# Kernel optimization log

Measured on AMD Instinct MI355X. Metric: run time of the kernel, lower is better.

The kernel has to match this reference:

```python
import jax, jax.numpy as jnp
import numpy as np

NUM_SUPERPIXELS = 256


def setup_inputs() -> dict:
    key = jax.random.key(0)
    k1, k2 = jax.random.split(key)
    B, H, W, C = 8, 512, 512, 64
    feature_map = jax.random.normal(k1, (B, H, W, C), dtype=jnp.float32)
    superpixel_map = jax.random.randint(k2, (B, H, W), 0, NUM_SUPERPIXELS, dtype=jnp.int32)
    return {"feature_map": feature_map, "superpixel_map": superpixel_map}


def reference(feature_map, superpixel_map):
    # feature_map: [B,H,W,C] float; superpixel_map: [B,H,W] int labels in [0, S)
    B, H, W, C = feature_map.shape
    S = NUM_SUPERPIXELS
    num_segments = B * S
    feat = feature_map.reshape(-1, C)                       # [B*H*W, C]
    batch_ids = jnp.arange(B, dtype=jnp.int32)[:, None, None]
    seg = (batch_ids * S + superpixel_map).reshape(-1)      # global segment id [B*H*W]
    sums = jax.ops.segment_sum(feat, seg, num_segments=num_segments)          # [B*S, C]
    counts = jax.ops.segment_sum(jnp.ones((seg.shape[0],), feat.dtype), seg,
                                 num_segments=num_segments)                    # [B*S]
    means = sums / jnp.maximum(counts, 1.0)[:, None]        # empty segments -> 0
    return means.reshape(B, S, C)
```

## Files before the change

kernel.cpp:

```cpp
#include <hip/hip_runtime.h>


#define NBATCH 8
#define NSEG 256
#define NCH 64
#define PPB (512 * 512)
#define BLOCKS_PER_BATCH 64
#define PIX_PER_BLOCK 4096
#define NWAVE 8
#define NCHUNK 16
#define CHUNK_PIX 256
#define QMAX 256
#define NROWS (NSEG + NWAVE)

__global__ __launch_bounds__(512, 4) void pool_kernel(const float* __restrict__ feat,
                                                      const int* __restrict__ sp,
                                                      float* __restrict__ outsum,
                                                      unsigned* __restrict__ cnts) {
    __shared__ float hist[NROWS * NCH];
    __shared__ unsigned cnt[NROWS];
    __shared__ int qd[NWAVE][QMAX];

    const int b = blockIdx.x >> 6;
    const int slab = blockIdx.x & 63;
    const int tid = threadIdx.x;
    const int lane = tid & 63;
    const int wave = tid >> 6;

    for (int i = tid; i < NROWS * NCH; i += 512) hist[i] = 0.0f;
    if (tid < NROWS) cnt[tid] = 0u;
    __syncthreads();

    const int pixbase = slab * PIX_PER_BLOCK;
    const int4* lp4 = (const int4*)(sp + (size_t)b * PPB + pixbase);
    const float* fb = feat + ((size_t)b * PPB + pixbase) * NCH + lane;

    const int dummy_e = (NSEG + wave) << 12;
    int* q = qd[wave];

    int4 lab = lp4[lane];
    for (int c = 0; c < NCHUNK; ++c) {
        const int cn = (c + 1 < NCHUNK) ? (c + 1) : c;
        int4 nlab = lp4[cn * 64 + lane];
        int qn = 0;
        const int pbase = c * CHUNK_PIX + 4 * lane;

#define PUSH(SV, CC)                                                          \
        {                                                                     \
            const int s_ = (SV);                                              \
            const bool own_ = ((s_ >> 5) == wave);                            \
            const unsigned long long m_ = __ballot(own_);                     \
            if (own_) {                                                       \
                const int r_ = __builtin_amdgcn_mbcnt_hi(                     \
                    (unsigned)(m_ >> 32),                                     \
                    __builtin_amdgcn_mbcnt_lo((unsigned)m_, 0));              \
                q[qn + r_] = (s_ << 12) | (pbase + (CC));                     \
            }                                                                 \
            qn += __builtin_popcountll(m_);                                   \
        }
        PUSH(lab.x, 0) PUSH(lab.y, 1) PUSH(lab.z, 2) PUSH(lab.w, 3)
#undef PUSH

        const int npad = (4 - (qn & 3)) & 3;
        if (lane < npad) q[qn + lane] = dummy_e;
        qn += npad;

        const int ng = qn >> 2;
        if (ng) {
            int4 eA = *(const int4*)&q[0];
            float fA0 = fb[(size_t)(eA.x & 4095) * NCH];
            float fA1 = fb[(size_t)(eA.y & 4095) * NCH];
            float fA2 = fb[(size_t)(eA.z & 4095) * NCH];
            float fA3 = fb[(size_t)(eA.w & 4095) * NCH];
            for (int g = 1; g < ng; ++g) {
                int4 eB = *(const int4*)&q[g * 4];
                float fB0 = fb[(size_t)(eB.x & 4095) * NCH];
                float fB1 = fb[(size_t)(eB.y & 4095) * NCH];
                float fB2 = fb[(size_t)(eB.z & 4095) * NCH];
                float fB3 = fb[(size_t)(eB.w & 4095) * NCH];

                hist[(eA.x >> 12) * NCH + lane] += fA0;
                if (lane == 0) cnt[eA.x >> 12]++;
                hist[(eA.y >> 12) * NCH + lane] += fA1;
                if (lane == 0) cnt[eA.y >> 12]++;
                hist[(eA.z >> 12) * NCH + lane] += fA2;
                if (lane == 0) cnt[eA.z >> 12]++;
                hist[(eA.w >> 12) * NCH + lane] += fA3;
                if (lane == 0) cnt[eA.w >> 12]++;

                eA = eB; fA0 = fB0; fA1 = fB1; fA2 = fB2; fA3 = fB3;
            }
            hist[(eA.x >> 12) * NCH + lane] += fA0;
            if (lane == 0) cnt[eA.x >> 12]++;
            hist[(eA.y >> 12) * NCH + lane] += fA1;
            if (lane == 0) cnt[eA.y >> 12]++;
            hist[(eA.z >> 12) * NCH + lane] += fA2;
            if (lane == 0) cnt[eA.z >> 12]++;
            hist[(eA.w >> 12) * NCH + lane] += fA3;
            if (lane == 0) cnt[eA.w >> 12]++;
        }
        lab = nlab;
    }
    __syncthreads();

    const size_t obase = (size_t)b * NSEG * NCH;
    for (int i = tid; i < NSEG * NCH; i += 512)
        unsafeAtomicAdd(&outsum[obase + i], hist[i]);
    if (tid < NSEG) atomicAdd(&cnts[(size_t)b * NSEG + tid], cnt[tid]);
}

__global__ void init_kernel(float* __restrict__ outsum, unsigned* __restrict__ cnts) {
    const int i = blockIdx.x * 256 + threadIdx.x;
    ((float4*)outsum)[i] = make_float4(0.f, 0.f, 0.f, 0.f);
    if (i < (NBATCH * NSEG) / 4) ((uint4*)cnts)[i] = make_uint4(0u, 0u, 0u, 0u);
}

__global__ void finalize_kernel(float* __restrict__ outsum,
                                const unsigned* __restrict__ cnts) {
    const int idx4 = blockIdx.x * blockDim.x + threadIdx.x;
    const unsigned c = cnts[idx4 >> 4];
    const float inv = 1.0f / (float)(c > 0u ? c : 1u);
    float4 v = ((float4*)outsum)[idx4];
    v.x *= inv; v.y *= inv; v.z *= inv; v.w *= inv;
    ((float4*)outsum)[idx4] = v;
}

extern "C" void kernel_launch(void* const* d_in, const int* in_sizes, int n_in,
                              void* d_out, int out_size, void* d_ws, size_t ws_size,
                              hipStream_t stream) {
    const float* feat = (const float*)d_in[0];
    const int* sp = (const int*)d_in[1];
    float* out = (float*)d_out;
    unsigned* cnts = (unsigned*)d_ws;
    (void)in_sizes; (void)n_in; (void)out_size; (void)ws_size;

    init_kernel<<<512, 256, 0, stream>>>(out, cnts);
    pool_kernel<<<NBATCH * BLOCKS_PER_BATCH, 512, 0, stream>>>(feat, sp, out, cnts);
    finalize_kernel<<<(NBATCH * NSEG * NCH / 4) / 256, 256, 0, stream>>>(out, cnts);
}
```

Baseline: 706.2 us.

## Replace global atomics with per-block partials and a separate reduce kernel

Each block now writes its shared-memory histogram and counts to its own workspace slot instead of atomically adding into the output. A new reduce kernel sums the 64 partials per batch and segment and divides by the count, which removes the init and finalize kernels. Counts are now taken with shared atomics at push time instead of per gathered element, and the gather loop is unrolled to 8 loads in flight. Launch bounds drop to 2 blocks per CU. The change trades global atomic contention for about 32 MB of extra workspace traffic plus a second pass, and relies on the workspace being large enough.

```diff
diff --git a/kernel.cpp b/kernel.cpp
--- a/kernel.cpp
+++ b/kernel.cpp
@@ -5,18 +5,18 @@
 #define NSEG 256
 #define NCH 64
 #define PPB (512 * 512)
-#define BLOCKS_PER_BATCH 64
+#define BPB 64
 #define PIX_PER_BLOCK 4096
 #define NWAVE 8
 #define NCHUNK 16
 #define CHUNK_PIX 256
-#define QMAX 256
+#define QMAX 264
 #define NROWS (NSEG + NWAVE)
 
-__global__ __launch_bounds__(512, 4) void pool_kernel(const float* __restrict__ feat,
+__global__ __launch_bounds__(512, 2) void pool_kernel(const float* __restrict__ feat,
                                                       const int* __restrict__ sp,
-                                                      float* __restrict__ outsum,
-                                                      unsigned* __restrict__ cnts) {
+                                                      float* __restrict__ pspart,
+                                                      unsigned* __restrict__ pscnt) {
     __shared__ float hist[NROWS * NCH];
     __shared__ unsigned cnt[NROWS];
     __shared__ int qd[NWAVE][QMAX];
@@ -27,7 +27,8 @@
     const int lane = tid & 63;
     const int wave = tid >> 6;
 
-    for (int i = tid; i < NROWS * NCH; i += 512) hist[i] = 0.0f;
+    for (int i = tid; i < (NROWS * NCH) / 4; i += 512)
+        ((float4*)hist)[i] = make_float4(0.f, 0.f, 0.f, 0.f);
     if (tid < NROWS) cnt[tid] = 0u;
     __syncthreads();
 
@@ -55,74 +56,91 @@
                     (unsigned)(m_ >> 32),                                     \
                     __builtin_amdgcn_mbcnt_lo((unsigned)m_, 0));              \
                 q[qn + r_] = (s_ << 12) | (pbase + (CC));                     \
+                atomicAdd(&cnt[s_], 1u);                                      \
             }                                                                 \
             qn += __builtin_popcountll(m_);                                   \
         }
         PUSH(lab.x, 0) PUSH(lab.y, 1) PUSH(lab.z, 2) PUSH(lab.w, 3)
 #undef PUSH
 
-        const int npad = (4 - (qn & 3)) & 3;
+        const int npad = (8 - (qn & 7)) & 7;
         if (lane < npad) q[qn + lane] = dummy_e;
         qn += npad;
 
-        const int ng = qn >> 2;
+        const int ng = qn >> 3;
         if (ng) {
-            int4 eA = *(const int4*)&q[0];
-            float fA0 = fb[(size_t)(eA.x & 4095) * NCH];
-            float fA1 = fb[(size_t)(eA.y & 4095) * NCH];
-            float fA2 = fb[(size_t)(eA.z & 4095) * NCH];
-            float fA3 = fb[(size_t)(eA.w & 4095) * NCH];
+            int4 a0 = *(const int4*)&q[0];
+            int4 a1 = *(const int4*)&q[4];
+            float f0 = fb[(size_t)(a0.x & 4095) * NCH];
+            float f1 = fb[(size_t)(a0.y & 4095) * NCH];
+            float f2 = fb[(size_t)(a0.z & 4095) * NCH];
+            float f3 = fb[(size_t)(a0.w & 4095) * NCH];
+            float f4 = fb[(size_t)(a1.x & 4095) * NCH];
+            float f5 = fb[(size_t)(a1.y & 4095) * NCH];
+            float f6 = fb[(size_t)(a1.z & 4095) * NCH];
+            float f7 = fb[(size_t)(a1.w & 4095) * NCH];
             for (int g = 1; g < ng; ++g) {
-                int4 eB = *(const int4*)&q[g * 4];
-                float fB0 = fb[(size_t)(eB.x & 4095) * NCH];
-                float fB1 = fb[(size_t)(eB.y & 4095) * NCH];
-                float fB2 = fb[(size_t)(eB.z & 4095) * NCH];
-                float fB3 = fb[(size_t)(eB.w & 4095) * NCH];
+                int4 b0 = *(const int4*)&q[g * 8];
+                int4 b1 = *(const int4*)&q[g * 8 + 4];
+                float h0 = fb[(size_t)(b0.x & 4095) * NCH];
+                float h1 = fb[(size_t)(b0.y & 4095) * NCH];
+                float h2 = fb[(size_t)(b0.z & 4095) * NCH];
+                float h3 = fb[(size_t)(b0.w & 4095) * NCH];
+                float h4 = fb[(size_t)(b1.x & 4095) * NCH];
+                float h5 = fb[(size_t)(b1.y & 4095) * NCH];
+                float h6 = fb[(size_t)(b1.z & 4095) * NCH];
+                float h7 = fb[(size_t)(b1.w & 4095) * NCH];
 
-                hist[(eA.x >> 12) * NCH + lane] += fA0;
-                if (lane == 0) cnt[eA.x >> 12]++;
-                hist[(eA.y >> 12) * NCH + lane] += fA1;
-                if (lane == 0) cnt[eA.y >> 12]++;
-                hist[(eA.z >> 12) * NCH + lane] += fA2;
-                if (lane == 0) cnt[eA.z >> 12]++;
-                hist[(eA.w >> 12) * NCH + lane] += fA3;
-                if (lane == 0) cnt[eA.w >> 12]++;
+                hist[(a0.x >> 12) * NCH + lane] += f0;
+                hist[(a0.y >> 12) * NCH + lane] += f1;
+                hist[(a0.z >> 12) * NCH + lane] += f2;
+                hist[(a0.w >> 12) * NCH + lane] += f3;
+                hist[(a1.x >> 12) * NCH + lane] += f4;
+                hist[(a1.y >> 12) * NCH + lane] += f5;
+                hist[(a1.z >> 12) * NCH + lane] += f6;
+                hist[(a1.w >> 12) * NCH + lane] += f7;
 
-                eA = eB; fA0 = fB0; fA1 = fB1; fA2 = fB2; fA3 = fB3;
+                a0 = b0; a1 = b1;
+                f0 = h0; f1 = h1; f2 = h2; f3 = h3;
+                f4 = h4; f5 = h5; f6 = h6; f7 = h7;
             }
-            hist[(eA.x >> 12) * NCH + lane] += fA0;
-            if (lane == 0) cnt[eA.x >> 12]++;
-            hist[(eA.y >> 12) * NCH + lane] += fA1;
-            if (lane == 0) cnt[eA.y >> 12]++;
-            hist[(eA.z >> 12) * NCH + lane] += fA2;
-            if (lane == 0) cnt[eA.z >> 12]++;
-            hist[(eA.w >> 12) * NCH + lane] += fA3;
-            if (lane == 0) cnt[eA.w >> 12]++;
+            hist[(a0.x >> 12) * NCH + lane] += f0;
+            hist[(a0.y >> 12) * NCH + lane] += f1;
+            hist[(a0.z >> 12) * NCH + lane] += f2;
+            hist[(a0.w >> 12) * NCH + lane] += f3;
+            hist[(a1.x >> 12) * NCH + lane] += f4;
+            hist[(a1.y >> 12) * NCH + lane] += f5;
+            hist[(a1.z >> 12) * NCH + lane] += f6;
+            hist[(a1.w >> 12) * NCH + lane] += f7;
         }
         lab = nlab;
     }
     __syncthreads();
 
-    const size_t obase = (size_t)b * NSEG * NCH;
-    for (int i = tid; i < NSEG * NCH; i += 512)
-        unsafeAtomicAdd(&outsum[obase + i], hist[i]);
-    if (tid < NSEG) atomicAdd(&cnts[(size_t)b * NSEG + tid], cnt[tid]);
+    float4* wp = (float4*)(pspart + (size_t)blockIdx.x * (NSEG * NCH));
+    const float4* hs = (const float4*)hist;
+    for (int i = tid; i < (NSEG * NCH) / 4; i += 512) wp[i] = hs[i];
+    if (tid < NSEG) pscnt[(size_t)blockIdx.x * NSEG + tid] = cnt[tid];
 }
 
-__global__ void init_kernel(float* __restrict__ outsum, unsigned* __restrict__ cnts) {
-    const int i = blockIdx.x * 256 + threadIdx.x;
-    ((float4*)outsum)[i] = make_float4(0.f, 0.f, 0.f, 0.f);
-    if (i < (NBATCH * NSEG) / 4) ((uint4*)cnts)[i] = make_uint4(0u, 0u, 0u, 0u);
-}
+__global__ __launch_bounds__(64) void reduce_kernel(const float* __restrict__ pspart,
+                                                    const unsigned* __restrict__ pscnt,
+                                                    float* __restrict__ out) {
+    const int bs = blockIdx.x;
+    const int bnum = bs >> 8;
+    const int seg = bs & 255;
+    const int lane = threadIdx.x;
 
-__global__ void finalize_kernel(float* __restrict__ outsum,
-                                const unsigned* __restrict__ cnts) {
-    const int idx4 = blockIdx.x * blockDim.x + threadIdx.x;
-    const unsigned c = cnts[idx4 >> 4];
-    const float inv = 1.0f / (float)(c > 0u ? c : 1u);
-    float4 v = ((float4*)outsum)[idx4];
-    v.x *= inv; v.y *= inv; v.z *= inv; v.w *= inv;
-    ((float4*)outsum)[idx4] = v;
+    const float* base = pspart + ((size_t)bnum * BPB * NSEG + seg) * NCH + lane;
+    float acc = 0.f;
+#pragma unroll
+    for (int s = 0; s < BPB; ++s)
+        acc += base[(size_t)s * NSEG * NCH];
+
+    unsigned c = pscnt[((size_t)bnum * BPB + lane) * NSEG + seg];
+    for (int o = 32; o; o >>= 1) c += __shfl_xor(c, o);
+
+    out[(size_t)bs * NCH + lane] = acc / (float)(c > 0u ? c : 1u);
 }
 
 extern "C" void kernel_launch(void* const* d_in, const int* in_sizes, int n_in,
@@ -131,10 +149,10 @@
     const float* feat = (const float*)d_in[0];
     const int* sp = (const int*)d_in[1];
     float* out = (float*)d_out;
-    unsigned* cnts = (unsigned*)d_ws;
+    float* pspart = (float*)d_ws;
+    unsigned* pscnt = (unsigned*)((char*)d_ws + (size_t)NBATCH * BPB * NSEG * NCH * 4);
     (void)in_sizes; (void)n_in; (void)out_size; (void)ws_size;
 
-    init_kernel<<<512, 256, 0, stream>>>(out, cnts);
-    pool_kernel<<<NBATCH * BLOCKS_PER_BATCH, 512, 0, stream>>>(feat, sp, out, cnts);
-    finalize_kernel<<<(NBATCH * NSEG * NCH / 4) / 256, 256, 0, stream>>>(out, cnts);
+    pool_kernel<<<NBATCH * BPB, 512, 0, stream>>>(feat, sp, pspart, pscnt);
+    reduce_kernel<<<NBATCH * NSEG, 64, 0, stream>>>(pspart, pscnt, out);
 }
```

Result: no change. 694.2 us (-1.7%).
